# Optimization experiments

Measured on AMD Instinct MI355X. Metric: run time of the kernel, lower is better.

The kernel has to match this reference:

```python
import jax, jax.numpy as jnp
import numpy as np

C = 128
NUM_GROUPS = 32  # min(32, 128 // 4)
EPS = 1e-6


def group_norm(x, gamma, beta):
    N, Cc, H, W = x.shape
    xg = x.reshape(N, NUM_GROUPS, -1)
    mean = xg.mean(axis=-1, keepdims=True)
    var = ((xg - mean) ** 2).mean(axis=-1, keepdims=True)
    xn = ((xg - mean) * jax.lax.rsqrt(var + EPS)).reshape(N, Cc, H, W)
    return xn * gamma[None, :, None, None] + beta[None, :, None, None]


def conv1x1(x, w, b):
    # w: [C_out, C_in], b: [C_out]; 1x1 conv == channel matmul
    return jnp.einsum('nchw,oc->nohw', x, w) + b[None, :, None, None]


def setup_inputs() -> dict:
    key = jax.random.key(0)
    ks = jax.random.split(key, 11)
    s = 1.0 / np.sqrt(C)
    return {
        'x': jax.random.normal(ks[0], (4, C, 64, 64), dtype=jnp.float32),
        'gamma': jnp.ones((C,), jnp.float32),
        'beta': jnp.zeros((C,), jnp.float32),
        'wq': jax.random.normal(ks[1], (C, C), jnp.float32) * s,
        'bq': jnp.zeros((C,), jnp.float32),
        'wk': jax.random.normal(ks[2], (C, C), jnp.float32) * s,
        'bk': jnp.zeros((C,), jnp.float32),
        'wv': jax.random.normal(ks[3], (C, C), jnp.float32) * s,
        'bv': jnp.zeros((C,), jnp.float32),
        'wo': jax.random.normal(ks[4], (C, C), jnp.float32) * s,
        'bo': jnp.zeros((C,), jnp.float32),
    }


def reference(x, gamma, beta, wq, bq, wk, bk, wv, bv, wo, bo):
    N, Cc, H, W = x.shape
    L = H * W
    xn = group_norm(x, gamma, beta)
    q = conv1x1(xn, wq, bq).reshape(N, Cc, L)  # [N,C,L]
    k = conv1x1(xn, wk, bk).reshape(N, Cc, L)
    v = conv1x1(xn, wv, bv).reshape(N, Cc, L)
    scale = 1.0 / jnp.sqrt(jnp.asarray(Cc, x.dtype))
    scores = jnp.einsum('ncl,ncm->nlm', q, k) * scale  # [N,L,L]
    weights = jax.nn.softmax(scores, axis=-1)
    attn = jnp.einsum('nlm,ncm->ncl', weights, v).reshape(N, Cc, H, W)
    return x + conv1x1(attn, wo, bo)
```

## Files before the change

### kernel.cpp

```cpp
#include <hip/hip_runtime.h>
#include <hip/hip_bf16.h>


#define N_B 4
#define C_D 128
#define L_D 4096
#define SPLIT 4
#define KVB 64
#define FSTEPS ((L_D/SPLIT)/KVB)
#define QSCALE (0.08838834764831845f * 1.4426950408889634f)
#define FIXM 16.0f

using f32x4  = __attribute__((ext_vector_type(4))) float;
using f32x16 = __attribute__((ext_vector_type(16))) float;
using bf16x8 = __attribute__((ext_vector_type(8))) short;

static __device__ __forceinline__ unsigned short f2bf(float f){
  return (unsigned short)((__builtin_bit_cast(unsigned int, f) + 0x8000u) >> 16);
}
static __device__ __forceinline__ float bf2f(unsigned short u){
  unsigned int x = ((unsigned int)u) << 16;
  return __builtin_bit_cast(float, x);
}
static __device__ __forceinline__ unsigned int pk2(float a, float b){
  unsigned int ua = __builtin_bit_cast(unsigned int, a) + 0x8000u;
  unsigned int ub = __builtin_bit_cast(unsigned int, b) + 0x8000u;
  return __builtin_amdgcn_perm(ub, ua, 0x07060302u);
}
static __device__ __forceinline__ float exp2a(float x){
  float r; asm("v_exp_f32 %0, %1" : "=v"(r) : "v"(x)); return r;
}
static __device__ __forceinline__ void gll16(const void* g, void* l){
  __builtin_amdgcn_global_load_lds(
      (const __attribute__((address_space(1))) unsigned int*)g,
      (__attribute__((address_space(3))) unsigned int*)l, 16, 0, 0);
}

__global__ __launch_bounds__(256) void gnw_k(
    const float* __restrict__ x, float* __restrict__ stats,
    const float* __restrict__ wq, const float* __restrict__ wk,
    const float* __restrict__ wv, const float* __restrict__ wo,
    unsigned short* __restrict__ wbf)
{
  int b = blockIdx.x, t = threadIdx.x;
  if (b >= 128){
    int b2 = b - 128;
    int mat = b2 >> 4;
    const float* src = (mat == 0) ? wq : (mat == 1) ? wk : (mat == 2) ? wv : wo;
    int off = (b2 & 15) * 1024 + t * 4;
    float4 v = *(const float4*)(src + off);
    *(uint2*)(wbf + mat*16384 + off) = make_uint2(pk2(v.x, v.y), pk2(v.z, v.w));
    return;
  }
  const float4* p = (const float4*)(x + (size_t)b * (4 * L_D));
  float s = 0.f, ss = 0.f;
#pragma unroll
  for (int i = 0; i < 16; ++i){
    float4 v = p[t + i*256];
    s  += v.x + v.y + v.z + v.w;
    ss += v.x*v.x + v.y*v.y + v.z*v.z + v.w*v.w;
  }
#pragma unroll
  for (int off = 32; off > 0; off >>= 1){
    s  += __shfl_down(s, off);
    ss += __shfl_down(ss, off);
  }
  __shared__ float rs4[4], rss4[4];
  if ((t & 63) == 0){ rs4[t>>6] = s; rss4[t>>6] = ss; }
  __syncthreads();
  if (t == 0){
    s  = rs4[0]+rs4[1]+rs4[2]+rs4[3];
    ss = rss4[0]+rss4[1]+rss4[2]+rss4[3];
    float mean = s * (1.f/16384.f);
    float var  = ss * (1.f/16384.f) - mean*mean;
    if (var < 0.f) var = 0.f;
    stats[2*b]   = mean;
    stats[2*b+1] = rsqrtf(var + 1e-6f);
  }
}

__global__ __launch_bounds__(256) void qkv_k(
    const float* __restrict__ x, const float* __restrict__ stats,
    const float* __restrict__ gamma, const float* __restrict__ beta,
    const unsigned short* __restrict__ wbf,
    const float* __restrict__ bq, const float* __restrict__ bk,
    const float* __restrict__ bv,
    unsigned short* __restrict__ q_ws, unsigned short* __restrict__ k_ws,
    unsigned short* __restrict__ v_ws)
{
  __shared__ unsigned short xnT[64][136];
  __shared__ unsigned short qbuf[64][136];

  int t = threadIdx.x, b = blockIdx.x;
  int n = b >> 6, l0 = (b & 63) * 64;

  {
    int l = t & 63, cq = t >> 6;
#pragma unroll
    for (int it = 0; it < 8; ++it){
      int c0 = cq*4 + it*16;
      int g  = c0 >> 2;
      float mean = stats[(n*32+g)*2];
      float rstd = stats[(n*32+g)*2+1];
      float vv[4];
#pragma unroll
      for (int jj = 0; jj < 4; ++jj){
        int c = c0 + jj;
        float sc = rstd * gamma[c];
        float bs = beta[c] - mean * sc;
        vv[jj] = x[(size_t)(n*C_D + c)*L_D + l0 + l]*sc + bs;
      }
      *(unsigned int*)&xnT[l][c0]   = pk2(vv[0], vv[1]);
      *(unsigned int*)&xnT[l][c0+2] = pk2(vv[2], vv[3]);
    }
  }
  __syncthreads();

  int w = t >> 6, lane = t & 63, u = lane >> 4, l15 = lane & 15;
  int wc = w >> 1, wl = w & 1;
  f32x4 zz = {0.f,0.f,0.f,0.f};

  for (int wi = 0; wi < 3; ++wi){
    const unsigned short* W = wbf + wi*16384;
    const float* Bv = (wi == 0) ? bq : (wi == 1) ? bk : bv;

    f32x4 acc[4][2];
#pragma unroll
    for (int ct = 0; ct < 4; ++ct)
#pragma unroll
      for (int lt = 0; lt < 2; ++lt) acc[ct][lt] = zz;

#pragma unroll
    for (int kst = 0; kst < 4; ++kst){
      bf16x8 bfrag[2];
#pragma unroll
      for (int lt = 0; lt < 2; ++lt)
        bfrag[lt] = *(const bf16x8*)&xnT[32*wl + 16*lt + l15][kst*32 + 8*u];
#pragma unroll
      for (int ct = 0; ct < 4; ++ct){
        bf16x8 af = *(const bf16x8*)(W + (size_t)(64*wc + 16*ct + l15)*C_D + kst*32 + 8*u);
#pragma unroll
        for (int lt = 0; lt < 2; ++lt)
          acc[ct][lt] = __builtin_amdgcn_mfma_f32_16x16x32_bf16(af, bfrag[lt], acc[ct][lt], 0, 0, 0);
      }
    }

    if (wi < 2){
      float qs = (wi == 0) ? QSCALE : 1.0f;
      __syncthreads();
#pragma unroll
      for (int ct = 0; ct < 4; ++ct){
        float bias[4];
#pragma unroll
        for (int r = 0; r < 4; ++r) bias[r] = Bv[64*wc + 16*ct + 4*u + r];
#pragma unroll
        for (int lt = 0; lt < 2; ++lt){
          float v0 = (acc[ct][lt][0] + bias[0]) * qs;
          float v1 = (acc[ct][lt][1] + bias[1]) * qs;
          float v2 = (acc[ct][lt][2] + bias[2]) * qs;
          float v3 = (acc[ct][lt][3] + bias[3]) * qs;
          int row = 32*wl + 16*lt + l15;
          int col = 64*wc + 16*ct + 4*u;
          *(unsigned int*)&qbuf[row][col]   = pk2(v0, v1);
          *(unsigned int*)&qbuf[row][col+2] = pk2(v2, v3);
        }
      }
      __syncthreads();
      {
        int l = t >> 2, ch = t & 3;
        unsigned short* dst = ((wi == 0) ? q_ws : k_ws) + (size_t)(n*L_D + l0 + l)*C_D + ch*32;
#pragma unroll
        for (int i = 0; i < 4; ++i)
          *(uint4*)(dst + i*8) = *(const uint4*)&qbuf[l][ch*32 + i*8];
      }
    } else {
      int p16 = (l15 & 3) | ((l15 & 4) << 1) | ((l15 & 8) >> 1);
#pragma unroll
      for (int ct = 0; ct < 4; ++ct){
        float bias[4];
#pragma unroll
        for (int r = 0; r < 4; ++r) bias[r] = Bv[64*wc + 16*ct + 4*u + r];
#pragma unroll
        for (int lt = 0; lt < 2; ++lt)
#pragma unroll
          for (int r = 0; r < 4; ++r){
            int co = 64*wc + 16*ct + 4*u + r;
            v_ws[(size_t)(n*C_D + co)*L_D + l0 + 32*wl + 16*lt + p16] =
                f2bf(acc[ct][lt][r] + bias[r]);
          }
      }
    }
  }
}

#define STEPBODY(STEP, SIN0, SIN1, SOUT0, SOUT1, DOQK)                           \
  {                                                                              \
    const int step_ = (STEP);                                                    \
    int pfi = step_ + 2; if (pfi > FSTEPS-1) pfi = FSTEPS-1;                     \
    int pbb = (step_ + 2) & 3;                                                   \
    {                                                                            \
      char* kN = shmem + (pbb << 14);                                            \
      char* vN = shmem + 65536 + (pbb << 14);                                    \
      gll16(kg[0] + (size_t)pfi*KVB*C_D, kN + ldof[0]);                          \
      gll16(kg[1] + (size_t)pfi*KVB*C_D, kN + ldof[1]);                          \
      gll16(vg[0] + pfi*KVB, vN + ldof[0]);                                      \
      gll16(vg[1] + pfi*KVB, vN + ldof[1]);                                      \
    }                                                                            \
    char* kB = shmem + ((step_ & 3) << 14);                                      \
    char* vP = shmem + 65536 + (((step_ - 1) & 3) << 14);                        \
    const bool doQK = (DOQK);                                                    \
    float p0[16], p1[16];                                                        \
    union Wu { unsigned int u[8]; bf16x8 h[2]; } Wm0, Wm1;                       \
    __builtin_amdgcn_s_setprio(1);                                               \
                                  \
    if (doQK){                                                                   \
      bf16x8 afr[8];                                                             \
      _Pragma("unroll")                                                          \
      for (int k = 0; k < 8; ++k)                                                \
        afr[k] = *(const bf16x8*)(kB + l31*256 +                                 \
                   ((32*k + 16*hi) ^ ((l31 & 15) << 4)));                        \
      SOUT0 = zz16;                                                              \
      _Pragma("unroll")                                                          \
      for (int k = 0; k < 8; ++k){                                               \
        SOUT0 = __builtin_amdgcn_mfma_f32_32x32x16_bf16(afr[k], qf[k], SOUT0, 0, 0, 0); \
        p0[2*k]   = exp2a(SIN0[2*k]   - FIXM);                                   \
        p0[2*k+1] = exp2a(SIN0[2*k+1] - FIXM);                                   \
      }                                                                          \
    } else {                                                                     \
      _Pragma("unroll")                                                          \
      for (int r = 0; r < 16; ++r) p0[r] = exp2a(SIN0[r] - FIXM);                \
    }                                                                            \
                                     \
    if (doQK){                                                                   \
      bf16x8 afr[8];                                                             \
      _Pragma("unroll")                                                          \
      for (int k = 0; k < 8; ++k)                                                \
        afr[k] = *(const bf16x8*)(kB + (32 + l31)*256 +                          \
                   ((32*k + 16*hi) ^ ((l31 & 15) << 4)));                        \
      SOUT1 = zz16;                                                              \
      _Pragma("unroll")                                                          \
      for (int k = 0; k < 8; ++k){                                               \
        SOUT1 = __builtin_amdgcn_mfma_f32_32x32x16_bf16(afr[k], qf[k], SOUT1, 0, 0, 0); \
        Wm0.u[k] = pk2(p0[2*k], p0[2*k+1]);                                      \
      }                                                                          \
    } else {                                                                     \
      _Pragma("unroll")                                                          \
      for (int k = 0; k < 8; ++k) Wm0.u[k] = pk2(p0[2*k], p0[2*k+1]);            \
    }                                                                            \
    rsum += (((p0[0]+p0[1])+(p0[2]+p0[3])) + ((p0[4]+p0[5])+(p0[6]+p0[7])))      \
          + (((p0[8]+p0[9])+(p0[10]+p0[11])) + ((p0[12]+p0[13])+(p0[14]+p0[15])));\
                                \
    _Pragma("unroll")                                                            \
    for (int sl = 0; sl < 2; ++sl){                                              \
      bf16x8 pfv = Wm0.h[sl];                                                    \
      bf16x8 vfr[4];                                                             \
      _Pragma("unroll")                                                          \
      for (int ct = 0; ct < 4; ++ct){                                            \
        int c = 32*ct + l31, vrow = c & 63;                                      \
        int lb = ((c >> 6) << 7) + 32*sl + 16*hi;                                \
        vfr[ct] = *(const bf16x8*)(vP + vrow*256 + (lb ^ ((vrow & 15) << 4)));   \
      }                                                                          \
      _Pragma("unroll")                                                          \
      for (int ct = 0; ct < 4; ++ct){                                            \
        accO[ct] = __builtin_amdgcn_mfma_f32_32x32x16_bf16(vfr[ct], pfv, accO[ct], 0, 0, 0); \
        p1[8*sl + 2*ct]     = exp2a(SIN1[8*sl + 2*ct]     - FIXM);               \
        p1[8*sl + 2*ct + 1] = exp2a(SIN1[8*sl + 2*ct + 1] - FIXM);               \
      }                                                                          \
    }                                                                            \
    _Pragma("unroll")                                                            \
    for (int k = 0; k < 8; ++k) Wm1.u[k] = pk2(p1[2*k], p1[2*k+1]);              \
    rsum += (((p1[0]+p1[1])+(p1[2]+p1[3])) + ((p1[4]+p1[5])+(p1[6]+p1[7])))      \
          + (((p1[8]+p1[9])+(p1[10]+p1[11])) + ((p1[12]+p1[13])+(p1[14]+p1[15])));\
                                                            \
    _Pragma("unroll")                                                            \
    for (int sl = 2; sl < 4; ++sl){                                              \
      bf16x8 pfv = Wm1.h[sl & 1];                                                \
      bf16x8 vfr[4];                                                             \
      _Pragma("unroll")                                                          \
      for (int ct = 0; ct < 4; ++ct){                                            \
        int c = 32*ct + l31, vrow = c & 63;                                      \
        int lb = ((c >> 6) << 7) + 32*sl + 16*hi;                                \
        vfr[ct] = *(const bf16x8*)(vP + vrow*256 + (lb ^ ((vrow & 15) << 4)));   \
      }                                                                          \
      _Pragma("unroll")                                                          \
      for (int ct = 0; ct < 4; ++ct)                                             \
        accO[ct] = __builtin_amdgcn_mfma_f32_32x32x16_bf16(vfr[ct], pfv, accO[ct], 0, 0, 0); \
    }                                                                            \
    __builtin_amdgcn_s_setprio(0);                                               \
    asm volatile("s_waitcnt vmcnt(4)" ::: "memory");                             \
    __builtin_amdgcn_s_barrier();                                                \
    asm volatile("" ::: "memory");                                               \
  }

__global__ __launch_bounds__(512, 2) void flash_split_k(
    const unsigned short* __restrict__ q_ws, const unsigned short* __restrict__ k_ws,
    const unsigned short* __restrict__ v_ws,
    unsigned short* __restrict__ po_ws, float* __restrict__ md_ws)
{
  __shared__ __align__(16) char shmem[131072];

  int t = threadIdx.x;
  int phys = blockIdx.x;
  int xcd = phys & 7, j = phys >> 3;
  int pair = xcd*8 + (j & 7);
  int s = j >> 3;
  int n = pair >> 4, lt256 = pair & 15;
  int l0 = lt256 * 256;
  int m_base = s * (L_D / SPLIT);
  int w = t >> 6, lane = t & 63, hi = lane >> 5, l31 = lane & 31;
  int lr = lane >> 4, ls = lane & 15;

  bf16x8 qf[8];
  {
    const unsigned short* qrow = q_ws + ((size_t)(n*L_D + l0 + 32*w + l31))*C_D;
#pragma unroll
    for (int kst = 0; kst < 8; ++kst)
      qf[kst] = *(const bf16x8*)(qrow + 16*kst + 8*hi);
  }

  f32x16 zz16;
#pragma unroll
  for (int i = 0; i < 16; ++i) zz16[i] = 0.f;
  f32x16 accO[4];
#pragma unroll
  for (int ct = 0; ct < 4; ++ct) accO[ct] = zz16;
  float rsum = 0.f;

  const unsigned short* kg[2];
  const unsigned short* vg[2];
  int ldof[2];
#pragma unroll
  for (int i = 0; i < 2; ++i){
    int row = 8*w + 4*i + lr;
    int ub = (ls << 4) ^ ((row & 15) << 4);
    kg[i] = k_ws + ((size_t)(n*L_D + m_base + row))*C_D + (ub >> 1);
    int c    = row + ((ub >> 7) << 6);
    int mloc = (ub & 127) >> 1;
    vg[i] = v_ws + ((size_t)(n*C_D + c))*L_D + m_base + mloc;
    ldof[i] = (8*w + 4*i)*256;
  }

#pragma unroll
  for (int pre = 0; pre < 3; ++pre){
    char* kD = shmem + (pre << 14);
    char* vD = shmem + 65536 + (pre << 14);
    gll16(kg[0] + (size_t)pre*KVB*C_D, kD + ldof[0]);
    gll16(kg[1] + (size_t)pre*KVB*C_D, kD + ldof[1]);
    gll16(vg[0] + pre*KVB, vD + ldof[0]);
    gll16(vg[1] + pre*KVB, vD + ldof[1]);
  }
  asm volatile("s_waitcnt vmcnt(4)" ::: "memory");
  __builtin_amdgcn_s_barrier();
  asm volatile("" ::: "memory");

  f32x16 sA0, sA1, sB0, sB1;
  {
    __builtin_amdgcn_s_setprio(1);
    sA0 = zz16; sA1 = zz16;
    bf16x8 afr[8];
#pragma unroll
    for (int k = 0; k < 8; ++k)
      afr[k] = *(const bf16x8*)(shmem + l31*256 + ((32*k + 16*hi) ^ ((l31 & 15) << 4)));
#pragma unroll
    for (int k = 0; k < 8; ++k)
      sA0 = __builtin_amdgcn_mfma_f32_32x32x16_bf16(afr[k], qf[k], sA0, 0, 0, 0);
#pragma unroll
    for (int k = 0; k < 8; ++k)
      afr[k] = *(const bf16x8*)(shmem + (32 + l31)*256 + ((32*k + 16*hi) ^ ((l31 & 15) << 4)));
#pragma unroll
    for (int k = 0; k < 8; ++k)
      sA1 = __builtin_amdgcn_mfma_f32_32x32x16_bf16(afr[k], qf[k], sA1, 0, 0, 0);
    __builtin_amdgcn_s_setprio(0);
  }

  for (int e = 1; e < 17; e += 2){
    STEPBODY(e,     sA0, sA1, sB0, sB1, true)
    STEPBODY(e + 1, sB0, sB1, sA0, sA1, (e + 1 < FSTEPS))
  }

  asm volatile("s_waitcnt vmcnt(0)" ::: "memory");
  __builtin_amdgcn_s_barrier();
  asm volatile("" ::: "memory");

  rsum += __shfl_xor(rsum, 32);

  char* tB = shmem;
  {
    int lloc = 32*w + l31;
    int tsw = (lloc & 15) << 4;
    char* tr = tB + (size_t)lloc*256;
#pragma unroll
    for (int ct = 0; ct < 4; ++ct)
#pragma unroll
      for (int q = 0; q < 4; ++q){
        int cb2 = 64*ct + 16*q + 8*hi;
        *(unsigned int*)(tr + ((cb2    ) ^ tsw)) = pk2(accO[ct][4*q+0], accO[ct][4*q+1]);
        *(unsigned int*)(tr + ((cb2 + 4) ^ tsw)) = pk2(accO[ct][4*q+2], accO[ct][4*q+3]);
      }
  }
  __syncthreads();
  {
    int row2 = t >> 1, hf2 = t & 1;
    int tile = row2 >> 7, lrow = row2 & 127;
    size_t pb = ((size_t)((n*32 + 2*lt256 + tile)*SPLIT + s)) * (size_t)(128*128);
    unsigned short* dst = po_ws + pb + (size_t)lrow*128 + hf2*64;
    const char* srcr = tB + row2*256;
    int sw2 = (row2 & 15) << 4;
#pragma unroll
    for (int i = 0; i < 8; ++i)
      *(uint4*)(dst + 8*i) = *(const uint4*)(srcr + ((hf2*128 + 16*i) ^ sw2));
  }
  if (lane < 32){
    int lg = 32*w + lane;
    int tile2 = lg >> 7, lrow2 = lg & 127;
    size_t mb2 = ((size_t)((n*32 + 2*lt256 + tile2)*SPLIT + s)) * 128;
    md_ws[mb2 + lrow2] = rsum;
  }
}

__global__ __launch_bounds__(256) void combine_k(
    const unsigned short* __restrict__ po_ws, const float* __restrict__ md_ws,
    const float* __restrict__ x, const unsigned short* __restrict__ wo_bf,
    const float* __restrict__ bo, float* __restrict__ out)
{
  __shared__ __align__(16) char aB[8192];

  int t = threadIdx.x, b = blockIdx.x;
  int xcd = b & 7, j = b >> 3;
  int pair = xcd*8 + (j & 7);
  int eighth = j >> 3;
  int n = pair >> 4, lt256 = pair & 15;
  int lt32 = lt256*8 + eighth;
  int f = lt32 >> 2;
  int loff = (lt32 & 3) * 32;
  int l0 = lt32 * 32;
  size_t pbase = ((size_t)((n*32 + f)*SPLIT)) * (size_t)(128*128);
  size_t mbase = ((size_t)((n*32 + f)*SPLIT)) * 128;

  {
    int l = t >> 3, q8 = t & 7;
    float Dg = 0.f;
#pragma unroll
    for (int s2 = 0; s2 < SPLIT; ++s2)
      Dg += md_ws[mbase + s2*128 + loff + l];
    float inv = 1.0f / Dg;

    float a[16];
#pragma unroll
    for (int i = 0; i < 16; ++i) a[i] = 0.f;
#pragma unroll
    for (int s2 = 0; s2 < SPLIT; ++s2){
      const uint4* p = (const uint4*)(po_ws + pbase + (size_t)s2*(128*128)
                                      + (size_t)(loff + l)*128 + q8*16);
#pragma unroll
      for (int i = 0; i < 2; ++i){
        uint4 uv = p[i];
        unsigned int uu[4] = {uv.x, uv.y, uv.z, uv.w};
#pragma unroll
        for (int j2 = 0; j2 < 4; ++j2){
          a[8*i + 2*j2]     += bf2f((unsigned short)(uu[j2] & 0xffffu));
          a[8*i + 2*j2 + 1] += bf2f((unsigned short)(uu[j2] >> 16));
        }
      }
    }
    char* ar = aB + l*256;
    int asw = (l & 7) << 4;
#pragma unroll
    for (int i = 0; i < 8; ++i){
      int cb = q8*32 + 4*i;
      *(unsigned int*)(ar + (cb ^ asw)) = pk2(a[2*i]*inv, a[2*i+1]*inv);
    }
  }
  __syncthreads();

  int w = t >> 6, lane = t & 63, hi = lane >> 5, l31 = lane & 31;
  f32x16 acc;
#pragma unroll
  for (int i = 0; i < 16; ++i) acc[i] = 0.f;

#pragma unroll
  for (int kst = 0; kst < 8; ++kst){
    bf16x8 bfg = *(const bf16x8*)(aB + l31*256 + ((32*kst + 16*hi) ^ ((l31 & 7) << 4)));
    bf16x8 af = *(const bf16x8*)(wo_bf + (size_t)(32*w + l31)*C_D + 16*kst + 8*hi);
    acc = __builtin_amdgcn_mfma_f32_32x32x16_bf16(af, bfg, acc, 0, 0, 0);
  }
#pragma unroll
  for (int r = 0; r < 16; ++r){
    int o = 32*w + (r & 3) + 8*(r >> 2) + 4*hi;
    size_t idx = (size_t)(n*C_D + o)*L_D + l0 + l31;
    out[idx] = x[idx] + bo[o] + acc[r];
  }
}

extern "C" void kernel_launch(void* const* d_in, const int* in_sizes, int n_in,
                              void* d_out, int out_size, void* d_ws, size_t ws_size,
                              hipStream_t stream) {
  const float* x     = (const float*)d_in[0];
  const float* gamma = (const float*)d_in[1];
  const float* beta  = (const float*)d_in[2];
  const float* wq    = (const float*)d_in[3];
  const float* bq    = (const float*)d_in[4];
  const float* wk    = (const float*)d_in[5];
  const float* bk    = (const float*)d_in[6];
  const float* wv    = (const float*)d_in[7];
  const float* bv    = (const float*)d_in[8];
  const float* wo    = (const float*)d_in[9];
  const float* bo    = (const float*)d_in[10];
  float* out = (float*)d_out;

  char* ws = (char*)d_ws;
  float* stats          = (float*)ws;
  unsigned short* q_ws  = (unsigned short*)(ws + 4096);
  unsigned short* k_ws  = q_ws + (size_t)N_B * L_D * C_D;
  unsigned short* v_ws  = k_ws + (size_t)N_B * L_D * C_D;
  unsigned short* po_ws = v_ws + (size_t)N_B * L_D * C_D;
  float* md_ws          = (float*)(po_ws + (size_t)N_B * 32 * SPLIT * 128 * 128);
  unsigned short* wbf   = (unsigned short*)(md_ws + (size_t)N_B * 32 * SPLIT * 128);

  gnw_k<<<192, 256, 0, stream>>>(x, stats, wq, wk, wv, wo, wbf);
  qkv_k<<<256, 256, 0, stream>>>(x, stats, gamma, beta, wbf, bq, bk, bv,
                                 q_ws, k_ws, v_ws);
  flash_split_k<<<256, 512, 0, stream>>>(q_ws, k_ws, v_ws, po_ws, md_ws);
  combine_k<<<512, 256, 0, stream>>>(po_ws, md_ws, x, wbf + 3*16384, bo, out);
}
```

Before: 72.71 us.

## Fuse split-K combine and output projection into flash kernel via atomic flags

Removes the separate combine kernel launch. Each flash block signals completion through an agent-scope atomic counter per query tile, spin-waits until all four splits of that tile are done, then combines the partial outputs for a 64-row slice and applies the wo projection plus residual. Flags are reset in the first kernel. This relies on all 256 blocks being co-resident (2 per CU) to avoid deadlock, and it adds spin-wait latency for whichever split finishes last.

```diff
diff --git a/kernel.cpp b/kernel.cpp
--- a/kernel.cpp
+++ b/kernel.cpp
@@ -40,11 +40,13 @@
     const float* __restrict__ x, float* __restrict__ stats,
     const float* __restrict__ wq, const float* __restrict__ wk,
     const float* __restrict__ wv, const float* __restrict__ wo,
-    unsigned short* __restrict__ wbf)
+    unsigned short* __restrict__ wbf, unsigned int* __restrict__ flags)
 {
   int b = blockIdx.x, t = threadIdx.x;
   if (b >= 128){
     int b2 = b - 128;
+    if (b2 == 0 && t < 64)
+      __hip_atomic_store(&flags[t], 0u, __ATOMIC_RELAXED, __HIP_MEMORY_SCOPE_AGENT);
     int mat = b2 >> 4;
     const float* src = (mat == 0) ? wq : (mat == 1) ? wk : (mat == 2) ? wv : wo;
     int off = (b2 & 15) * 1024 + t * 4;
@@ -295,7 +297,10 @@
 __global__ __launch_bounds__(512, 2) void flash_split_k(
     const unsigned short* __restrict__ q_ws, const unsigned short* __restrict__ k_ws,
     const unsigned short* __restrict__ v_ws,
-    unsigned short* __restrict__ po_ws, float* __restrict__ md_ws)
+    unsigned short* __restrict__ po_ws, float* __restrict__ md_ws,
+    const float* __restrict__ x, const unsigned short* __restrict__ wo_bf,
+    const float* __restrict__ bo, float* __restrict__ out,
+    unsigned int* __restrict__ flags)
 {
   __shared__ __align__(16) char shmem[131072];
 
@@ -416,79 +421,77 @@
     size_t mb2 = ((size_t)((n*32 + 2*lt256 + tile2)*SPLIT + s)) * 128;
     md_ws[mb2 + lrow2] = rsum;
   }
-}
-
-__global__ __launch_bounds__(256) void combine_k(
-    const unsigned short* __restrict__ po_ws, const float* __restrict__ md_ws,
-    const float* __restrict__ x, const unsigned short* __restrict__ wo_bf,
-    const float* __restrict__ bo, float* __restrict__ out)
-{
-  __shared__ __align__(16) char aB[8192];
-
-  int t = threadIdx.x, b = blockIdx.x;
-  int xcd = b & 7, j = b >> 3;
-  int pair = xcd*8 + (j & 7);
-  int eighth = j >> 3;
-  int n = pair >> 4, lt256 = pair & 15;
-  int lt32 = lt256*8 + eighth;
-  int f = lt32 >> 2;
-  int loff = (lt32 & 3) * 32;
-  int l0 = lt32 * 32;
-  size_t pbase = ((size_t)((n*32 + f)*SPLIT)) * (size_t)(128*128);
-  size_t mbase = ((size_t)((n*32 + f)*SPLIT)) * 128;
+
+  __syncthreads();
+  if (t == 0){
+    __threadfence();
+    __hip_atomic_fetch_add(&flags[pair], 1u, __ATOMIC_RELEASE, __HIP_MEMORY_SCOPE_AGENT);
+    while (__hip_atomic_load(&flags[pair], __ATOMIC_ACQUIRE, __HIP_MEMORY_SCOPE_AGENT) < 4u) {}
+  }
+  __syncthreads();
 
   {
-    int l = t >> 3, q8 = t & 7;
-    float Dg = 0.f;
-#pragma unroll
-    for (int s2 = 0; s2 < SPLIT; ++s2)
-      Dg += md_ws[mbase + s2*128 + loff + l];
-    float inv = 1.0f / Dg;
-
-    float a[16];
-#pragma unroll
-    for (int i = 0; i < 16; ++i) a[i] = 0.f;
-#pragma unroll
-    for (int s2 = 0; s2 < SPLIT; ++s2){
-      const uint4* p = (const uint4*)(po_ws + pbase + (size_t)s2*(128*128)
-                                      + (size_t)(loff + l)*128 + q8*16);
-#pragma unroll
-      for (int i = 0; i < 2; ++i){
-        uint4 uv = p[i];
-        unsigned int uu[4] = {uv.x, uv.y, uv.z, uv.w};
-#pragma unroll
-        for (int j2 = 0; j2 < 4; ++j2){
-          a[8*i + 2*j2]     += bf2f((unsigned short)(uu[j2] & 0xffffu));
-          a[8*i + 2*j2 + 1] += bf2f((unsigned short)(uu[j2] >> 16));
+    int lt64 = lt256*4 + s;
+    int f2 = lt64 >> 1, loff = (lt64 & 1)*64, l0c = lt64*64;
+    size_t pbase = ((size_t)((n*32 + f2)*SPLIT)) * (size_t)(128*128);
+    size_t mbase = ((size_t)((n*32 + f2)*SPLIT)) * 128;
+    char* aB = shmem;
+
+    {
+      int l = t >> 3, q8 = t & 7;
+      float Dg = 0.f;
+#pragma unroll
+      for (int s2 = 0; s2 < SPLIT; ++s2)
+        Dg += md_ws[mbase + s2*128 + loff + l];
+      float inv = 1.0f / Dg;
+
+      float a[16];
+#pragma unroll
+      for (int i = 0; i < 16; ++i) a[i] = 0.f;
+#pragma unroll
+      for (int s2 = 0; s2 < SPLIT; ++s2){
+        const uint4* p = (const uint4*)(po_ws + pbase + (size_t)s2*(128*128)
+                                        + (size_t)(loff + l)*128 + q8*16);
+#pragma unroll
+        for (int i = 0; i < 2; ++i){
+          uint4 uv = p[i];
+          unsigned int uu[4] = {uv.x, uv.y, uv.z, uv.w};
+#pragma unroll
+          for (int j2 = 0; j2 < 4; ++j2){
+            a[8*i + 2*j2]     += bf2f((unsigned short)(uu[j2] & 0xffffu));
+            a[8*i + 2*j2 + 1] += bf2f((unsigned short)(uu[j2] >> 16));
+          }
         }
       }
+      char* ar = aB + l*256;
+      int asw = (l & 7) << 4;
+#pragma unroll
+      for (int i = 0; i < 8; ++i){
+        int cb = q8*32 + 4*i;
+        *(unsigned int*)(ar + (cb ^ asw)) = pk2(a[2*i]*inv, a[2*i+1]*inv);
+      }
     }
-    char* ar = aB + l*256;
-    int asw = (l & 7) << 4;
-#pragma unroll
-    for (int i = 0; i < 8; ++i){
-      int cb = q8*32 + 4*i;
-      *(unsigned int*)(ar + (cb ^ asw)) = pk2(a[2*i]*inv, a[2*i+1]*inv);
+    __syncthreads();
+
+    {
+      int ow = w & 3, lh2 = w >> 2;
+      f32x16 acc;
+#pragma unroll
+      for (int i = 0; i < 16; ++i) acc[i] = 0.f;
+#pragma unroll
+      for (int kst = 0; kst < 8; ++kst){
+        int row = 32*lh2 + l31;
+        bf16x8 bfg = *(const bf16x8*)(aB + row*256 + ((32*kst + 16*hi) ^ ((row & 7) << 4)));
+        bf16x8 af = *(const bf16x8*)(wo_bf + (size_t)(32*ow + l31)*C_D + 16*kst + 8*hi);
+        acc = __builtin_amdgcn_mfma_f32_32x32x16_bf16(af, bfg, acc, 0, 0, 0);
+      }
+#pragma unroll
+      for (int r = 0; r < 16; ++r){
+        int o = 32*ow + (r & 3) + 8*(r >> 2) + 4*hi;
+        size_t idx = (size_t)(n*C_D + o)*L_D + l0c + 32*lh2 + l31;
+        out[idx] = x[idx] + bo[o] + acc[r];
+      }
     }
-  }
-  __syncthreads();
-
-  int w = t >> 6, lane = t & 63, hi = lane >> 5, l31 = lane & 31;
-  f32x16 acc;
-#pragma unroll
-  for (int i = 0; i < 16; ++i) acc[i] = 0.f;
-
-#pragma unroll
-  for (int kst = 0; kst < 8; ++kst){
-    bf16x8 bfg = *(const bf16x8*)(aB + l31*256 + ((32*kst + 16*hi) ^ ((l31 & 7) << 4)));
-    bf16x8 af = *(const bf16x8*)(wo_bf + (size_t)(32*w + l31)*C_D + 16*kst + 8*hi);
-    acc = __builtin_amdgcn_mfma_f32_32x32x16_bf16(af, bfg, acc, 0, 0, 0);
-  }
-#pragma unroll
-  for (int r = 0; r < 16; ++r){
-    int o = 32*w + (r & 3) + 8*(r >> 2) + 4*hi;
-    size_t idx = (size_t)(n*C_D + o)*L_D + l0 + l31;
-    out[idx] = x[idx] + bo[o] + acc[r];
   }
 }
 
@@ -516,10 +519,11 @@
   unsigned short* po_ws = v_ws + (size_t)N_B * L_D * C_D;
   float* md_ws          = (float*)(po_ws + (size_t)N_B * 32 * SPLIT * 128 * 128);
   unsigned short* wbf   = (unsigned short*)(md_ws + (size_t)N_B * 32 * SPLIT * 128);
-
-  gnw_k<<<192, 256, 0, stream>>>(x, stats, wq, wk, wv, wo, wbf);
+  unsigned int* flags   = (unsigned int*)(wbf + 4*16384);
+
+  gnw_k<<<192, 256, 0, stream>>>(x, stats, wq, wk, wv, wo, wbf, flags);
   qkv_k<<<256, 256, 0, stream>>>(x, stats, gamma, beta, wbf, bq, bk, bv,
                                  q_ws, k_ws, v_ws);
-  flash_split_k<<<256, 512, 0, stream>>>(q_ws, k_ws, v_ws, po_ws, md_ws);
-  combine_k<<<512, 256, 0, stream>>>(po_ws, md_ws, x, wbf + 3*16384, bo, out);
-}
+  flash_split_k<<<256, 512, 0, stream>>>(q_ws, k_ws, v_ws, po_ws, md_ws,
+                                         x, wbf + 3*16384, bo, out, flags);
+}
```

Result: slower. 89.13 us (+22.6%).
